# Performance work log

Hardware: AMD Instinct MI355X
Metric: run time of the kernel (lower is better)

The kernel has to match this reference:

```python
import jax, jax.numpy as jnp
import numpy as np

N = 3072
R = 16
B = 16


def setup_inputs() -> dict:
    key = jax.random.key(0)
    k1, k2, k3, k4, k5 = jax.random.split(key, 5)
    z1 = jax.random.normal(k1, (N, R), dtype=jnp.float32)
    z2 = jax.random.normal(k2, (N, R), dtype=jnp.float32)
    seg_matrix = jax.random.randint(k3, (N, N), 0, 2).astype(jnp.float32)
    cls_label = jax.random.randint(k4, (N,), 0, 30).astype(jnp.int64)
    batch = jnp.sort(jax.random.randint(k5, (N,), 0, B)).astype(jnp.int64)
    return {"z1": z1, "z2": z2, "seg_matrix": seg_matrix,
            "cls_label": cls_label, "batch": batch}


def reference(z1, z2, seg_matrix, cls_label, batch):
    n, r = z1.shape
    # seg_matrix += eye(N): self-pairs never have seg == 0
    seg = seg_matrix + jnp.eye(n, dtype=seg_matrix.dtype)
    # nodes with class labels 24/25/26 are excluded
    node_mask = (cls_label != 24) & (cls_label != 25) & (cls_label != 26)
    # pair (i, j) is written iff both nodes valid, same graph, and seg[i,j] == 0.
    # (the per-batch meshgrid/nonzero loop == same-batch pair condition)
    pair = (node_mask[:, None] & node_mask[None, :]
            & (batch[:, None] == batch[None, :])
            & (seg == 0.0))                              # [N, N]
    # default value: one-hot on relation 0 (concat of ones and zeros)
    default = jax.nn.one_hot(0, r, dtype=z1.dtype)        # [R]
    prod = z1[:, None, :] * z2[None, :, :]                # [N, N, R]
    return jnp.where(pair[:, :, None], prod, default)
```

## Files before the change

kernel.cpp:

```cpp
#include <hip/hip_runtime.h>
#include <cstddef>

#define NN 3072
#define RR 16
#define UNROLL 8

typedef float f32x4 __attribute__((ext_vector_type(4)));

__global__ void frd_key_kernel(const int* __restrict__ cls,
                               const int* __restrict__ batch,
                               int* __restrict__ key) {
    int i = blockIdx.x * blockDim.x + threadIdx.x;
    if (i < NN) {
        int c = cls[i];
        bool valid = (c != 24) && (c != 25) && (c != 26);
        key[i] = valid ? batch[i] : -1;
    }
}

__global__ __launch_bounds__(256)
void frd_main_kernel(const float* __restrict__ z1,
                     const float* __restrict__ z2,
                     const float* __restrict__ seg,
                     const int* __restrict__ key,
                     float* __restrict__ out) {
    const int base = blockIdx.x * (256 * UNROLL) + threadIdx.x;
    const float d0 = ((threadIdx.x & 3) == 0) ? 1.0f : 0.0f;

#pragma unroll
    for (int k = 0; k < UNROLL; ++k) {
        const int idx = base + k * 256;
        const int pair = idx >> 2;
        const int q = idx & 3;
        const int i = pair / NN;
        const int j = pair - i * NN;

        const float s = seg[pair];
        const int ki = key[i];
        const int kj = key[j];
        const float seg_eff = s + ((i == j) ? 1.0f : 0.0f);
        const bool is_pair = (ki == kj) && (ki >= 0) && (seg_eff == 0.0f);

        const float4 a = *reinterpret_cast<const float4*>(z1 + i * RR + q * 4);
        const float4 b = *reinterpret_cast<const float4*>(z2 + j * RR + q * 4);

        f32x4 r;
        r.x = is_pair ? a.x * b.x : d0;
        r.y = is_pair ? a.y * b.y : 0.0f;
        r.z = is_pair ? a.z * b.z : 0.0f;
        r.w = is_pair ? a.w * b.w : 0.0f;

        __builtin_nontemporal_store(r, reinterpret_cast<f32x4*>(out + (size_t)idx * 4));
    }
}

extern "C" void kernel_launch(void* const* d_in, const int* in_sizes, int n_in,
                              void* d_out, int out_size, void* d_ws, size_t ws_size,
                              hipStream_t stream) {
    const float* z1  = (const float*)d_in[0];
    const float* z2  = (const float*)d_in[1];
    const float* seg = (const float*)d_in[2];
    const int* cls   = (const int*)d_in[3];
    const int* batch = (const int*)d_in[4];
    float* out = (float*)d_out;
    int* key = (int*)d_ws;

    frd_key_kernel<<<(NN + 255) / 256, 256, 0, stream>>>(cls, batch, key);

    const int total = NN * NN * 4;
    frd_main_kernel<<<total / (256 * UNROLL), 256, 0, stream>>>(z1, z2, seg, key, out);
}
```

Before: 122.3 us.

## Split into default fill and per-batch diagonal-block kernel to skip seg reads

Replaces the single fused kernel with a fill kernel that writes the default one-hot only for pairs outside valid same-batch blocks, plus a diagonal-block kernel that scans only same-batch column ranges using precomputed batch start offsets. This avoids reading the full N×N seg matrix and the z1/z2 loads for pairs that cannot be active. It relies on batch being sorted, adds a third launch, and the diag kernel has uneven per-row work and partial-block divergence.

```diff
diff --git a/kernel.cpp b/kernel.cpp
--- a/kernel.cpp
+++ b/kernel.cpp
@@ -3,54 +3,78 @@
 
 #define NN 3072
 #define RR 16
+#define NB 16
 #define UNROLL 8
 
 typedef float f32x4 __attribute__((ext_vector_type(4)));
 
-__global__ void frd_key_kernel(const int* __restrict__ cls,
-                               const int* __restrict__ batch,
-                               int* __restrict__ key) {
-    int i = blockIdx.x * blockDim.x + threadIdx.x;
-    if (i < NN) {
-        int c = cls[i];
-        bool valid = (c != 24) && (c != 25) && (c != 26);
-        key[i] = valid ? batch[i] : -1;
+__global__ void frd_prep_kernel(const int* __restrict__ cls,
+                                const int* __restrict__ batch,
+                                int* __restrict__ key,
+                                int* __restrict__ start) {
+    int t = blockIdx.x * blockDim.x + threadIdx.x;
+    if (t < NN) {
+        int c = cls[t];
+        int b = batch[t];
+        key[t] = (c != 24 && c != 25 && c != 26) ? b : -1;
+        int prev = (t == 0) ? -1 : batch[t - 1];
+        for (int bb = prev + 1; bb <= b; ++bb) start[bb] = t;
+        if (t == NN - 1)
+            for (int bb = b + 1; bb <= NB; ++bb) start[bb] = NN;
     }
 }
 
 __global__ __launch_bounds__(256)
-void frd_main_kernel(const float* __restrict__ z1,
-                     const float* __restrict__ z2,
-                     const float* __restrict__ seg,
-                     const int* __restrict__ key,
-                     float* __restrict__ out) {
+void frd_fill_kernel(const int* __restrict__ key, float* __restrict__ out) {
     const int base = blockIdx.x * (256 * UNROLL) + threadIdx.x;
-    const float d0 = ((threadIdx.x & 3) == 0) ? 1.0f : 0.0f;
+    const int q = threadIdx.x & 3;
+    const f32x4 val = {(q == 0) ? 1.0f : 0.0f, 0.0f, 0.0f, 0.0f};
 
 #pragma unroll
     for (int k = 0; k < UNROLL; ++k) {
         const int idx = base + k * 256;
         const int pair = idx >> 2;
-        const int q = idx & 3;
         const int i = pair / NN;
         const int j = pair - i * NN;
-
-        const float s = seg[pair];
         const int ki = key[i];
         const int kj = key[j];
+        const bool skip = (ki >= 0) && (ki == kj);
+        if (!skip)
+            __builtin_nontemporal_store(val, reinterpret_cast<f32x4*>(out + (size_t)idx * 4));
+    }
+}
+
+__global__ __launch_bounds__(256)
+void frd_diag_kernel(const float* __restrict__ z1,
+                     const float* __restrict__ z2,
+                     const float* __restrict__ seg,
+                     const int* __restrict__ key,
+                     const int* __restrict__ start,
+                     float* __restrict__ out) {
+    const int i = blockIdx.x;
+    const int ki = key[i];
+    if (ki < 0) return;
+    const int s0 = start[ki];
+    const int s1 = start[ki + 1];
+    const int q = threadIdx.x & 3;
+    const int g = threadIdx.x >> 2;
+
+    const float4 a = *reinterpret_cast<const float4*>(z1 + i * RR + q * 4);
+    const float d0 = (q == 0) ? 1.0f : 0.0f;
+
+    for (int j = s0 + g; j < s1; j += 64) {
+        if (key[j] != ki) continue;
+        const float s = seg[i * NN + j];
         const float seg_eff = s + ((i == j) ? 1.0f : 0.0f);
-        const bool is_pair = (ki == kj) && (ki >= 0) && (seg_eff == 0.0f);
-
-        const float4 a = *reinterpret_cast<const float4*>(z1 + i * RR + q * 4);
-        const float4 b = *reinterpret_cast<const float4*>(z2 + j * RR + q * 4);
-
+        float* op = out + ((size_t)i * NN + j) * RR + q * 4;
         f32x4 r;
-        r.x = is_pair ? a.x * b.x : d0;
-        r.y = is_pair ? a.y * b.y : 0.0f;
-        r.z = is_pair ? a.z * b.z : 0.0f;
-        r.w = is_pair ? a.w * b.w : 0.0f;
-
-        __builtin_nontemporal_store(r, reinterpret_cast<f32x4*>(out + (size_t)idx * 4));
+        if (seg_eff == 0.0f) {
+            const float4 b = *reinterpret_cast<const float4*>(z2 + j * RR + q * 4);
+            r.x = a.x * b.x; r.y = a.y * b.y; r.z = a.z * b.z; r.w = a.w * b.w;
+        } else {
+            r.x = d0; r.y = 0.0f; r.z = 0.0f; r.w = 0.0f;
+        }
+        __builtin_nontemporal_store(r, reinterpret_cast<f32x4*>(op));
     }
 }
 
@@ -63,10 +87,11 @@
     const int* cls   = (const int*)d_in[3];
     const int* batch = (const int*)d_in[4];
     float* out = (float*)d_out;
-    int* key = (int*)d_ws;
+    int* key   = (int*)d_ws;
+    int* start = key + NN;
 
-    frd_key_kernel<<<(NN + 255) / 256, 256, 0, stream>>>(cls, batch, key);
-
+    frd_prep_kernel<<<(NN + 255) / 256, 256, 0, stream>>>(cls, batch, key, start);
     const int total = NN * NN * 4;
-    frd_main_kernel<<<total / (256 * UNROLL), 256, 0, stream>>>(z1, z2, seg, key, out);
+    frd_fill_kernel<<<total / (256 * UNROLL), 256, 0, stream>>>(key, out);
+    frd_diag_kernel<<<NN, 256, 0, stream>>>(z1, z2, seg, key, start, out);
 }
```

Measured after the change: 126.7 us. 3.6% more time.
